# Optimization experiments

Measured on AMD Instinct MI355X. Metric: run time of the kernel, lower is better.

## Reference

```python
import jax, jax.numpy as jnp
import numpy as np

B, N, D, DFC, EMB, L = 16, 1024, 128, 128, 64, 4
NHOPS = (1, 2, 3, 4)  # tatic='cont': nhop(i) = i + 1
EDGE_P = 0.03


def _make_adj(k):
    u = jax.random.uniform(k, (B, N, N))
    a = u < EDGE_P
    a = a | jnp.transpose(a, (0, 2, 1))          # undirected
    a = a | jnp.eye(N, dtype=bool)[None]         # self loops
    return a.astype(jnp.float32)


def setup_inputs() -> dict:
    key = jax.random.key(0)
    ks = jax.random.split(key, 16)
    s = 0.05
    x = jax.random.normal(ks[0], (B, N, 2 * EMB), jnp.float32)
    adj1 = _make_adj(ks[1])
    adj2 = _make_adj(ks[2])
    valid = jnp.ones((B, N), jnp.float32)
    embede_w = jax.random.normal(ks[3], (D, 2 * EMB)) * s
    gW = jax.random.normal(ks[4], (L, D, D)) * s
    gb = jnp.zeros((L, D), jnp.float32)
    gA = jax.random.normal(ks[5], (L, D, D)) * s
    gate_w = jax.random.normal(ks[6], (L, 1, 2 * D)) * s
    gate_b = jnp.zeros((L, 1), jnp.float32)
    fc0_w = jax.random.normal(ks[7], (DFC, D)) * s
    fc0_b = jnp.zeros((DFC,), jnp.float32)
    fc1_w = jax.random.normal(ks[8], (DFC, DFC)) * s
    fc1_b = jnp.zeros((DFC,), jnp.float32)
    fc2_w = jax.random.normal(ks[9], (DFC, DFC)) * s
    fc2_b = jnp.zeros((DFC,), jnp.float32)
    fc3_w = jax.random.normal(ks[10], (1, DFC)) * s
    fc3_b = jnp.zeros((1,), jnp.float32)
    return dict(x=x, adj1=adj1, adj2=adj2, valid=valid, embede_w=embede_w,
                gW=gW, gb=gb, gA=gA, gate_w=gate_w, gate_b=gate_b,
                fc0_w=fc0_w, fc0_b=fc0_b, fc1_w=fc1_w, fc1_b=fc1_b,
                fc2_w=fc2_w, fc2_b=fc2_b, fc3_w=fc3_w, fc3_b=fc3_b)


def _glema(x, adj, W, b, A, gw, gbias, nhop):
    h = x @ W.T + b                                        # [B,N,D]
    e = jnp.einsum('bjl,bkl->bjk', jnp.einsum('bjd,de->bje', h, A), h)
    e = e + jnp.transpose(e, (0, 2, 1))                    # undirected
    att = jnp.where(adj > 0, e, jnp.float32(0.0))
    att = jax.nn.softmax(att, axis=1) * adj                # softmax over dim 1, then adj mask
    az = jax.nn.relu(jnp.einsum('bij,bjd->bid', att, h))
    coeff = jax.nn.sigmoid(jnp.concatenate([h, az], -1) @ gw.T + gbias)  # [B,N,1]
    z = h
    for _ in range(nhop):
        az = jax.nn.relu(jnp.einsum('bij,bjd->bid', att, z))
        z = coeff * h + (1.0 - coeff) * az
    return z


def reference(x, adj1, adj2, valid, embede_w, gW, gb, gA, gate_w, gate_b,
              fc0_w, fc0_b, fc1_w, fc1_b, fc2_w, fc2_b, fc3_w, fc3_b):
    h = x @ embede_w.T                                     # embede (no bias)
    for k in range(L):                                     # branch='both': c_hs2 - c_hs1
        h1 = _glema(h, adj1, gW[k], gb[k], gA[k], gate_w[k], gate_b[k], NHOPS[k])
        h2 = _glema(h, adj2, gW[k], gb[k], gA[k], gate_w[k], gate_b[k], NHOPS[k])
        h = h2 - h1                                        # dropout p used in eval mode -> identity
    h = h * valid[..., None]
    pooled = h.sum(1) / valid.sum(1, keepdims=True)        # [B,D]
    y = jax.nn.relu(pooled @ fc0_w.T + fc0_b)
    y = jax.nn.relu(y @ fc1_w.T + fc1_b)
    y = jax.nn.relu(y @ fc2_w.T + fc2_b)
    y = jax.nn.sigmoid(y @ fc3_w.T + fc3_b)
    return y.reshape(-1)                                   # [B]
```

## Files before the change

kernel.cpp:

```cpp
#include <hip/hip_runtime.h>

typedef _Float16 half_t;
typedef _Float16 half8 __attribute__((ext_vector_type(8)));
typedef _Float16 half4v __attribute__((ext_vector_type(4)));
typedef float floatx4 __attribute__((ext_vector_type(4)));

#define MFMA(a,b,c) __builtin_amdgcn_mfma_f32_16x16x32_f16(a,b,c,0,0,0)

#define NB 16
#define NLEN 1024
#define DD 128
#define BN (NB*NLEN)
#define BND ((size_t)NB*NLEN*DD)
#define BNN ((size_t)NB*NLEN*NLEN)
#define ELLS 128
#define EMP 1044

static __device__ inline half_t f16h(unsigned pk) {
    unsigned short us = (unsigned short)(pk & 0xffffu);
    half_t h; __builtin_memcpy(&h, &us, 2); return h;
}

__global__ __launch_bounds__(256)
void k_pre(const float* __restrict__ adj1, const float* __restrict__ adj2,
           unsigned* __restrict__ ell, unsigned* __restrict__ cntA,
           const float* __restrict__ x, const float* __restrict__ Ew, half_t* __restrict__ h16,
           const float* __restrict__ gW, const float* __restrict__ gA,
           half_t* __restrict__ Wf, half_t* __restrict__ STf) {
    int tid = threadIdx.x;
    int bid = blockIdx.x;
    if (bid < 8192) {
        __shared__ unsigned ebuf[4][ELLS];
        int w = tid >> 6, l = tid & 63;
        int R = bid * 4 + w;
        int br = R >> 14, nb = R & 16383;
        const float* arow = (br ? adj2 : adj1) + (size_t)nb * 1024;
        unsigned* myb = ebuf[w];
        myb[l] = 0u; myb[l + 64] = 0u;
        float4 v0 = *(const float4*)&arow[l * 4];
        float4 v1 = *(const float4*)&arow[256 + l * 4];
        float4 v2 = *(const float4*)&arow[512 + l * 4];
        float4 v3 = *(const float4*)&arow[768 + l * 4];
        unsigned long long lmask = (l == 0) ? 0ull : (~0ull >> (64 - l));
        int base = 0;
        float vals[16] = {v0.x, v0.y, v0.z, v0.w, v1.x, v1.y, v1.z, v1.w,
                          v2.x, v2.y, v2.z, v2.w, v3.x, v3.y, v3.z, v3.w};
#pragma unroll
        for (int ch = 0; ch < 4; ch++) {
#pragma unroll
            for (int comp = 0; comp < 4; comp++) {
                bool pred = vals[ch * 4 + comp] > 0.f;
                unsigned long long b = __ballot(pred);
                if (pred) {
                    int idx = base + __popcll(b & lmask);
                    if (idx < ELLS) myb[idx] = ((unsigned)(ch * 256 + l * 4 + comp)) << 16;
                }
                base += __popcll(b);
            }
        }
        if (base > ELLS) base = ELLS;
        if (l == 0) cntA[R] = (unsigned)base;
        uint2 o = {myb[l * 2], myb[l * 2 + 1]};
        *(uint2*)&ell[(size_t)R * ELLS + l * 2] = o;
        return;
    }
    if (bid >= 10240) {
        int i = (bid - 10240) * 256 + tid;
        Wf[i] = (half_t)gW[i];
        int base = i & ~16383;
        int lrem = i & 16383;
        int d = lrem >> 7, e = lrem & 127;
        STf[base + (e << 7) + d] = (half_t)(gA[i] + gA[base + (e << 7) + d]);
        return;
    }
    __shared__ float rows[8][DD];
    int g = (bid - 8192) * 8;
    {
        int nl = tid >> 5, c4 = (tid & 31) * 4;
        *(float4*)&rows[nl][c4] = *(const float4*)&x[(size_t)(g + nl) * DD + c4];
    }
    __syncthreads();
    int t = tid & 127, half = tid >> 7;
    const float* wr = Ew + (size_t)t * DD;
    float acc[4] = {0.f, 0.f, 0.f, 0.f};
    for (int k = 0; k < DD; k++) {
        float w = wr[k];
#pragma unroll
        for (int m = 0; m < 4; m++) acc[m] += rows[half + 2 * m][k] * w;
    }
#pragma unroll
    for (int m = 0; m < 4; m++) h16[(size_t)(g + half + 2 * m) * DD + t] = (half_t)acc[m];
}

__global__ __launch_bounds__(256)
void k_proj(const half_t* __restrict__ pa, const half_t* __restrict__ pb,
            const half_t* __restrict__ Wf, const float* __restrict__ bias,
            const half_t* __restrict__ STf,
            half_t* __restrict__ hbr16, half_t* __restrict__ hbrF, half_t* __restrict__ hSF) {
    __shared__ half_t htile[32 * 136];
    __shared__ half_t hbtile[32 * 136];
    int g = blockIdx.x * 32;
    int t = threadIdx.x;
    int w = t >> 6, l = t & 63, q = l >> 4, l15 = l & 15;
#pragma unroll
    for (int v = 0; v < 2; v++) {
        int idx = v * 256 + t; int r = idx >> 4, c8 = (idx & 15) * 8;
        half8 va = *(const half8*)&pa[((size_t)(g + r) << 7) + c8];
        if (pb) {
            half8 vb = *(const half8*)&pb[((size_t)(g + r) << 7) + c8];
            va = va - vb;
        }
        *(half8*)&htile[r * 136 + c8] = va;
    }
    __syncthreads();
    int rowh = (w & 1) * 16;
    int c0 = (w >> 1) * 4;
    half8 a1[4];
#pragma unroll
    for (int kc = 0; kc < 4; kc++) a1[kc] = *(const half8*)&htile[(rowh + l15) * 136 + kc * 32 + q * 8];
    floatx4 acc[4];
#pragma unroll
    for (int cc = 0; cc < 4; cc++) {
        int col = (c0 + cc) * 16 + l15;
        floatx4 a = {0.f, 0.f, 0.f, 0.f};
#pragma unroll
        for (int kc = 0; kc < 4; kc++) {
            half8 bf = *(const half8*)&Wf[((size_t)col << 7) + kc * 32 + q * 8];
            a = MFMA(a1[kc], bf, a);
        }
        float bv = bias[col];
        a.x += bv; a.y += bv; a.z += bv; a.w += bv;
        acc[cc] = a;
    }
#pragma unroll
    for (int cc = 0; cc < 4; cc++) {
        int col = (c0 + cc) * 16 + l15;
#pragma unroll
        for (int r = 0; r < 4; r++)
            hbtile[(rowh + q * 4 + r) * 136 + col] = (half_t)acc[cc][r];
    }
    __syncthreads();
    half8 a2[4];
#pragma unroll
    for (int kc = 0; kc < 4; kc++) a2[kc] = *(const half8*)&hbtile[(rowh + l15) * 136 + kc * 32 + q * 8];
#pragma unroll
    for (int cc = 0; cc < 4; cc++) {
        int col = (c0 + cc) * 16 + l15;
        floatx4 a = {0.f, 0.f, 0.f, 0.f};
#pragma unroll
        for (int kc = 0; kc < 4; kc++) {
            half8 bf = *(const half8*)&STf[((size_t)col << 7) + kc * 32 + q * 8];
            a = MFMA(a2[kc], bf, a);
        }
        acc[cc] = a;
    }
    __syncthreads();
#pragma unroll
    for (int cc = 0; cc < 4; cc++) {
        int col = (c0 + cc) * 16 + l15;
#pragma unroll
        for (int r = 0; r < 4; r++) htile[(rowh + q * 4 + r) * 136 + col] = (half_t)acc[cc][r];
    }
    __syncthreads();
#pragma unroll
    for (int v = 0; v < 2; v++) {
        int idx = v * 256 + t; int r = idx >> 4, c8 = (idx & 15) * 8;
        *(half8*)&hbr16[((size_t)(g + r) << 7) + c8] = *(const half8*)&hbtile[r * 136 + c8];
    }
#pragma unroll
    for (int v = 0; v < 2; v++) {
        int fi = v * 256 + t;
        int g2 = fi >> 8, kc = (fi >> 6) & 3, li = fi & 63;
        int src = (g2 * 16 + (li & 15)) * 136 + kc * 32 + (li >> 4) * 8;
        size_t dst = (((size_t)(blockIdx.x * 2 + g2) * 4 + kc) << 10) + li * 8;
        *(half8*)&hbrF[dst] = *(const half8*)&hbtile[src];
        *(half8*)&hSF[dst]  = *(const half8*)&htile[src];
    }
}

__global__ __launch_bounds__(256)
void k_E(const half_t* __restrict__ hSF, const half_t* __restrict__ hbrF,
         const half_t* __restrict__ hbr16,
         unsigned* __restrict__ ell, const unsigned* __restrict__ cntA,
         float* __restrict__ rsr, half_t* __restrict__ hbrs) {
    int b = blockIdx.y, s = blockIdx.x;
    int t = threadIdx.x, w = t >> 6, l = t & 63, q = l >> 4, l15 = l & 15;
    __shared__ half_t emS[16 * EMP];
    __shared__ float rsS[2][16];
    size_t Gb = (size_t)b * 64;
    half8 A[4];
#pragma unroll
    for (int kc = 0; kc < 4; kc++)
        A[kc] = *(const half8*)&hSF[(((Gb + s) * 4 + kc) << 10) + l * 8];
#pragma unroll 4
    for (int cg = 0; cg < 16; cg++) {
        int c0 = w * 256 + cg * 16;
        floatx4 a = {0.f, 0.f, 0.f, 0.f};
#pragma unroll
        for (int kc = 0; kc < 4; kc++) {
            half8 bf = *(const half8*)&hbrF[(((Gb + w * 16 + cg) * 4 + kc) << 10) + l * 8];
            a = MFMA(A[kc], bf, a);
        }
#pragma unroll
        for (int r = 0; r < 4; r++)
            emS[(q * 4 + r) * EMP + c0 + l15] = (half_t)a[r];
    }
    __syncthreads();
    const float CN = 0.000335462627903f;
#pragma unroll
    for (int rr = 0; rr < 4; rr++) {
        int rl = w * 4 + rr;
        int rowg = b * 1024 + s * 16 + rl;
#pragma unroll
        for (int br = 0; br < 2; br++) {
            size_t R = ((size_t)br << 14) + rowg;
            int cn = (int)cntA[R];
            float rs = 0.f;
            for (int base = 0; base < cn; base += 64) {
                int si = base + l;
                float v = 0.f;
                if (si < cn) {
                    unsigned pk = ell[R * ELLS + si];
                    int col = (int)(pk >> 16);
                    float em = (float)emS[rl * EMP + col];
                    v = __expf(em - 8.f);
                    half_t hv = (half_t)v;
                    unsigned short us; __builtin_memcpy(&us, &hv, 2);
                    ((unsigned short*)ell)[(R * ELLS + si) * 2] = us;
                }
                rs += v;
            }
            rs += __shfl_xor(rs, 1); rs += __shfl_xor(rs, 2);
            rs += __shfl_xor(rs, 4); rs += __shfl_xor(rs, 8);
            rs += __shfl_xor(rs, 16); rs += __shfl_xor(rs, 32);
            if (l == 0) {
                float rv = 1.f / (rs + (1024.f - (float)cn) * CN);
                rsr[R] = rv;
                rsS[br][rl] = rv;
            }
        }
    }
    __syncthreads();
    const half_t* hrow = hbr16 + ((size_t)b << 17) + ((size_t)(s * 16) << 7);
#pragma unroll
    for (int v = 0; v < 2; v++) {
        int idx = v * 256 + t;
        int row = idx >> 5, br2 = (idx >> 4) & 1, ch = idx & 15;
        half8 hv = *(const half8*)&hrow[(size_t)row * 128 + ch * 8];
        float sc = rsS[br2][row];
        half8 o;
#pragma unroll
        for (int d = 0; d < 8; d++) o[d] = (half_t)(sc * (float)hv[d]);
        *(half8*)&hbrs[(size_t)br2 * BND + ((size_t)(b * 1024 + s * 16 + row) << 7) + ch * 8] = o;
    }
}

__global__ __launch_bounds__(256)
void k_az(const unsigned* __restrict__ ell, const unsigned* __restrict__ cntA,
          const float* __restrict__ rsr,
          const half_t* __restrict__ zin, const half_t* __restrict__ hbr16,
          const float* __restrict__ gw, const float* __restrict__ gb_,
          float* __restrict__ cfb, half_t* __restrict__ outp, int mode) {
    int t = threadIdx.x, w = t >> 6, l = t & 63;
    int g = l >> 4, l15 = l & 15;
    int R = blockIdx.x * 16 + w * 4 + g;
    int br = R >> 14, nb = R & 16383;
    const unsigned* ep = ell + (size_t)R * ELLS;
    int cn = (int)cntA[R];
    const half_t* zb = zin + (size_t)br * BND + (((size_t)(nb & ~1023)) << 7) + l15 * 8;
    half8 acc8 = {};
    uint4 p4 = *(const uint4*)ep;
    for (int s = 0; s < cn; s += 4) {
        uint4 cur = p4;
        p4 = *(const uint4*)(ep + s + 4);
        unsigned pk[4] = {cur.x, cur.y, cur.z, cur.w};
#pragma unroll
        for (int i = 0; i < 4; i++) {
            half8 zz = *(const half8*)(zb + (((size_t)(pk[i] >> 16)) << 7));
            half_t hv = f16h(pk[i]);
            half8 vv = {hv, hv, hv, hv, hv, hv, hv, hv};
            acc8 += zz * vv;
        }
    }
    float acc[8];
#pragma unroll
    for (int d = 0; d < 8; d++) acc[d] = fmaxf((float)acc8[d], 0.f);
    half8 hv8 = *(const half8*)&hbr16[((size_t)nb << 7) + l15 * 8];
    float hv[8];
#pragma unroll
    for (int d = 0; d < 8; d++) hv[d] = (float)hv8[d];
    float cf;
    if (mode >= 3) {
        const float* g1 = gw + l15 * 8;
        const float* g2 = gw + 128 + l15 * 8;
        float dp = 0.f;
#pragma unroll
        for (int d = 0; d < 8; d++) dp += hv[d] * g1[d] + acc[d] * g2[d];
        dp += __shfl_xor(dp, 1); dp += __shfl_xor(dp, 2);
        dp += __shfl_xor(dp, 4); dp += __shfl_xor(dp, 8);
        cf = 1.f / (1.f + __expf(-(dp + gb_[0])));
        if (l15 == 0) cfb[R] = cf;
    } else {
        cf = cfb[R];
    }
    float sc = (mode == 1 || mode == 3) ? rsr[R] : 1.f;
    half8 o;
#pragma unroll
    for (int d = 0; d < 8; d++)
        o[d] = (half_t)(sc * (cf * hv[d] + (1.f - cf) * acc[d]));
    *(half8*)&outp[(size_t)R * DD + l15 * 8] = o;
}

__global__ __launch_bounds__(256)
void k_pool(const half_t* __restrict__ z2, const half_t* __restrict__ z1,
            const float* __restrict__ valid, float* __restrict__ part) {
    int b = blockIdx.y, s = blockIdx.x;
    int t = threadIdx.x, d = t & 127, hf = t >> 7;
    __shared__ float red[128];
    float acc = 0.f;
    int nbase = s * 128 + hf * 64;
    for (int n = nbase; n < nbase + 64; n++) {
        size_t gi = ((size_t)(b * 1024 + n) << 7) + d;
        acc += ((float)z2[gi] - (float)z1[gi]) * valid[b * 1024 + n];
    }
    if (hf) red[d] = acc;
    __syncthreads();
    if (!hf) part[(b * 8 + s) * 128 + d] = acc + red[d];
}

__global__ __launch_bounds__(128)
void k_mlp(const float* __restrict__ part, const float* __restrict__ valid,
           const float* __restrict__ w0, const float* __restrict__ b0,
           const float* __restrict__ w1, const float* __restrict__ b1,
           const float* __restrict__ w2, const float* __restrict__ b2,
           const float* __restrict__ w3, const float* __restrict__ b3,
           float* __restrict__ out) {
    int b = blockIdx.x, t = threadIdx.x;
    __shared__ float y0[DD], y1[DD];
    __shared__ float sred[2];
    float vs = 0.f;
    for (int n = t; n < NLEN; n += 128) vs += valid[b * NLEN + n];
    for (int off = 32; off; off >>= 1) vs += __shfl_down(vs, off);
    if ((t & 63) == 0) sred[t >> 6] = vs;
    __syncthreads();
    float vsum = sred[0] + sred[1];
    float acc = 0.f;
#pragma unroll
    for (int s = 0; s < 8; s++) acc += part[(b * 8 + s) * 128 + t];
    y0[t] = acc / vsum;
    __syncthreads();
    float a = b0[t];
    for (int k = 0; k < DD; k++) a += y0[k] * w0[t * DD + k];
    y1[t] = fmaxf(a, 0.f);
    __syncthreads();
    a = b1[t];
    for (int k = 0; k < DD; k++) a += y1[k] * w1[t * DD + k];
    y0[t] = fmaxf(a, 0.f);
    __syncthreads();
    a = b2[t];
    for (int k = 0; k < DD; k++) a += y0[k] * w2[t * DD + k];
    y1[t] = fmaxf(a, 0.f);
    __syncthreads();
    float p = y1[t] * w3[t];
    for (int off = 32; off; off >>= 1) p += __shfl_down(p, off);
    if ((t & 63) == 0) sred[t >> 6] = p;
    __syncthreads();
    if (t == 0) out[b] = 1.f / (1.f + __expf(-(sred[0] + sred[1] + b3[0])));
}

extern "C" void kernel_launch(void* const* d_in, const int* in_sizes, int n_in,
                              void* d_out, int out_size, void* d_ws, size_t ws_size,
                              hipStream_t stream) {
    (void)in_sizes; (void)n_in; (void)out_size; (void)ws_size;
    const float* x     = (const float*)d_in[0];
    const float* adj1  = (const float*)d_in[1];
    const float* adj2  = (const float*)d_in[2];
    const float* valid = (const float*)d_in[3];
    const float* Ew    = (const float*)d_in[4];
    const float* gW    = (const float*)d_in[5];
    const float* gb    = (const float*)d_in[6];
    const float* gA    = (const float*)d_in[7];
    const float* gatew = (const float*)d_in[8];
    const float* gateb = (const float*)d_in[9];
    const float* w0 = (const float*)d_in[10]; const float* b0 = (const float*)d_in[11];
    const float* w1 = (const float*)d_in[12]; const float* b1 = (const float*)d_in[13];
    const float* w2 = (const float*)d_in[14]; const float* b2 = (const float*)d_in[15];
    const float* w3 = (const float*)d_in[16]; const float* b3 = (const float*)d_in[17];
    float* out = (float*)d_out;

    char* p = (char*)d_ws;
    float* rsr  = (float*)p; p += 2 * BN * 4;
    float* cfb  = (float*)p; p += 2 * BN * 4;
    float* partb = (float*)p; p += (size_t)NB * 8 * 128 * 4;
    half_t* h16   = (half_t*)p; p += BND * 2;
    half_t* hbr16 = (half_t*)p; p += BND * 2;
    half_t* hbrF  = (half_t*)p; p += BND * 2;
    half_t* hSF   = (half_t*)p; p += BND * 2;
    half_t* hbrs  = (half_t*)p; p += 2 * BND * 2;
    half_t* zf    = (half_t*)p; p += 2 * BND * 2;
    half_t* zsA   = (half_t*)p; p += 2 * BND * 2;
    half_t* zsB   = (half_t*)p; p += 2 * BND * 2;
    unsigned* ell = (unsigned*)p; p += (size_t)2 * BN * ELLS * 4 + 16;
    unsigned* cntA = (unsigned*)p; p += (size_t)2 * BN * 4;
    half_t* Wf16 = (half_t*)p; p += (size_t)4 * 128 * 128 * 2;
    half_t* ST16 = (half_t*)p; p += (size_t)4 * 128 * 128 * 2;

    k_pre<<<10496, 256, 0, stream>>>(adj1, adj2, ell, cntA, x, Ew, h16, gW, gA, Wf16, ST16);

    for (int k = 0; k < 4; k++) {
        int nhop = k + 1;
        const half_t* pa = k ? (zf + BND) : h16;
        const half_t* pb = k ? zf : nullptr;
        k_proj<<<512, 256, 0, stream>>>(pa, pb, Wf16 + (size_t)k * 16384, gb + k * 128,
                                        ST16 + (size_t)k * 16384, hbr16, hbrF, hSF);
        k_E<<<dim3(64, NB), 256, 0, stream>>>(hSF, hbrF, hbr16, ell, cntA, rsr, hbrs);
        half_t* tgate = (nhop == 1) ? zf : zsA;
        k_az<<<2048, 256, 0, stream>>>(ell, cntA, rsr, hbrs, hbr16,
                                       gatew + k * 256, gateb + k, cfb, tgate,
                                       (nhop == 1) ? 4 : 3);
        half_t* src = tgate;
        for (int hop = 2; hop <= nhop; hop++) {
            half_t* dst = (hop == nhop) ? zf : ((hop & 1) ? zsA : zsB);
            k_az<<<2048, 256, 0, stream>>>(ell, cntA, rsr, src, hbr16,
                                           gatew + k * 256, gateb + k, cfb, dst,
                                           (hop == nhop) ? 2 : 1);
            src = dst;
        }
    }
    k_pool<<<dim3(8, NB), 256, 0, stream>>>(zf + BND, zf, valid, partb);
    k_mlp<<<16, 128, 0, stream>>>(partb, valid, w0, b0, w1, b1, w2, b2, w3, b3, out);
}
```

Before: 696.0 us.

## Rework ELL compaction, vectorize embed matvec, swizzle block order, split az accumulators

```diff
diff --git a/kernel.cpp b/kernel.cpp
--- a/kernel.cpp
+++ b/kernel.cpp
@@ -41,25 +41,29 @@
         float4 v1 = *(const float4*)&arow[256 + l * 4];
         float4 v2 = *(const float4*)&arow[512 + l * 4];
         float4 v3 = *(const float4*)&arow[768 + l * 4];
-        unsigned long long lmask = (l == 0) ? 0ull : (~0ull >> (64 - l));
-        int base = 0;
         float vals[16] = {v0.x, v0.y, v0.z, v0.w, v1.x, v1.y, v1.z, v1.w,
                           v2.x, v2.y, v2.z, v2.w, v3.x, v3.y, v3.z, v3.w};
-#pragma unroll
-        for (int ch = 0; ch < 4; ch++) {
-#pragma unroll
-            for (int comp = 0; comp < 4; comp++) {
-                bool pred = vals[ch * 4 + comp] > 0.f;
-                unsigned long long b = __ballot(pred);
-                if (pred) {
-                    int idx = base + __popcll(b & lmask);
-                    if (idx < ELLS) myb[idx] = ((unsigned)(ch * 256 + l * 4 + comp)) << 16;
-                }
-                base += __popcll(b);
-            }
-        }
-        if (base > ELLS) base = ELLS;
-        if (l == 0) cntA[R] = (unsigned)base;
+        unsigned m = 0u;
+#pragma unroll
+        for (int i = 0; i < 16; i++) m |= (vals[i] > 0.f) ? (1u << i) : 0u;
+        int cnt = __popc(m);
+        int pre = cnt;
+#pragma unroll
+        for (int off = 1; off < 64; off <<= 1) {
+            int o = __shfl_up(pre, off);
+            if (l >= off) pre += o;
+        }
+        int total = __shfl(pre, 63);
+        int idx = pre - cnt;
+        unsigned mm = m;
+        while (mm) {
+            int i = __builtin_ctz(mm);
+            mm &= mm - 1;
+            if (idx < ELLS)
+                myb[idx] = ((unsigned)(((i >> 2) << 8) + l * 4 + (i & 3))) << 16;
+            idx++;
+        }
+        if (l == 0) cntA[R] = (unsigned)(total > ELLS ? ELLS : total);
         uint2 o = {myb[l * 2], myb[l * 2 + 1]};
         *(uint2*)&ell[(size_t)R * ELLS + l * 2] = o;
         return;
@@ -81,15 +85,19 @@
     }
     __syncthreads();
     int t = tid & 127, half = tid >> 7;
-    const float* wr = Ew + (size_t)t * DD;
+    const float4* wr4 = (const float4*)(Ew + (size_t)t * DD);
     float acc[4] = {0.f, 0.f, 0.f, 0.f};
-    for (int k = 0; k < DD; k++) {
-        float w = wr[k];
-#pragma unroll
-        for (int m = 0; m < 4; m++) acc[m] += rows[half + 2 * m][k] * w;
-    }
-#pragma unroll
-    for (int m = 0; m < 4; m++) h16[(size_t)(g + half + 2 * m) * DD + t] = (half_t)acc[m];
+#pragma unroll 8
+    for (int k4 = 0; k4 < 32; k4++) {
+        float4 wv = wr4[k4];
+#pragma unroll
+        for (int mi = 0; mi < 4; mi++) {
+            float4 rv = *(const float4*)&rows[half + 2 * mi][k4 * 4];
+            acc[mi] += rv.x * wv.x + rv.y * wv.y + rv.z * wv.z + rv.w * wv.w;
+        }
+    }
+#pragma unroll
+    for (int mi = 0; mi < 4; mi++) h16[(size_t)(g + half + 2 * mi) * DD + t] = (half_t)acc[mi];
 }
 
 __global__ __launch_bounds__(256)
@@ -183,7 +191,9 @@
          const half_t* __restrict__ hbr16,
          unsigned* __restrict__ ell, const unsigned* __restrict__ cntA,
          float* __restrict__ rsr, half_t* __restrict__ hbrs) {
-    int b = blockIdx.y, s = blockIdx.x;
+    int hw = blockIdx.y * 64 + blockIdx.x;
+    int wk = (hw & 7) * 128 + (hw >> 3);
+    int b = wk >> 6, s = wk & 63;
     int t = threadIdx.x, w = t >> 6, l = t & 63, q = l >> 4, l15 = l & 15;
     __shared__ half_t emS[16 * EMP];
     __shared__ float rsS[2][16];
@@ -263,28 +273,35 @@
           float* __restrict__ cfb, half_t* __restrict__ outp, int mode) {
     int t = threadIdx.x, w = t >> 6, l = t & 63;
     int g = l >> 4, l15 = l & 15;
-    int R = blockIdx.x * 16 + w * 4 + g;
+    int bid = blockIdx.x;
+    int wk = (bid & 7) * 256 + (bid >> 3);
+    int R = wk * 16 + w * 4 + g;
     int br = R >> 14, nb = R & 16383;
     const unsigned* ep = ell + (size_t)R * ELLS;
     int cn = (int)cntA[R];
     const half_t* zb = zin + (size_t)br * BND + (((size_t)(nb & ~1023)) << 7) + l15 * 8;
-    half8 acc8 = {};
+    half8 acc8a = {}, acc8b = {};
     uint4 p4 = *(const uint4*)ep;
     for (int s = 0; s < cn; s += 4) {
         uint4 cur = p4;
         p4 = *(const uint4*)(ep + s + 4);
-        unsigned pk[4] = {cur.x, cur.y, cur.z, cur.w};
-#pragma unroll
-        for (int i = 0; i < 4; i++) {
-            half8 zz = *(const half8*)(zb + (((size_t)(pk[i] >> 16)) << 7));
-            half_t hv = f16h(pk[i]);
-            half8 vv = {hv, hv, hv, hv, hv, hv, hv, hv};
-            acc8 += zz * vv;
-        }
+        half8 z0 = *(const half8*)(zb + (((size_t)(cur.x >> 16)) << 7));
+        half8 z1 = *(const half8*)(zb + (((size_t)(cur.y >> 16)) << 7));
+        half8 z2 = *(const half8*)(zb + (((size_t)(cur.z >> 16)) << 7));
+        half8 z3 = *(const half8*)(zb + (((size_t)(cur.w >> 16)) << 7));
+        half_t h0 = f16h(cur.x), h1 = f16h(cur.y), h2 = f16h(cur.z), h3 = f16h(cur.w);
+        half8 s0 = {h0,h0,h0,h0,h0,h0,h0,h0};
+        half8 s1 = {h1,h1,h1,h1,h1,h1,h1,h1};
+        half8 s2 = {h2,h2,h2,h2,h2,h2,h2,h2};
+        half8 s3 = {h3,h3,h3,h3,h3,h3,h3,h3};
+        acc8a += z0 * s0;
+        acc8b += z1 * s1;
+        acc8a += z2 * s2;
+        acc8b += z3 * s3;
     }
     float acc[8];
 #pragma unroll
-    for (int d = 0; d < 8; d++) acc[d] = fmaxf((float)acc8[d], 0.f);
+    for (int d = 0; d < 8; d++) acc[d] = fmaxf((float)acc8a[d] + (float)acc8b[d], 0.f);
     half8 hv8 = *(const half8*)&hbr16[((size_t)nb << 7) + l15 * 8];
     float hv[8];
 #pragma unroll
```

After: 678.9 us. 1.03x faster.
